# Kernel optimization log

Hardware: AMD Instinct MI355X
Metric: run time of the kernel (lower is better)

The kernel has to match this reference:

```python
import jax, jax.numpy as jnp
import numpy as np
from jax import lax

B, C, T, H, HEAD, NC = 256, 64, 2048, 64, 32, 8

def setup_inputs() -> dict:
    key = jax.random.key(0)
    ks = jax.random.split(key, 20)
    s = 0.08
    d = {}
    d["x"] = jax.random.normal(ks[0], (B, C, T), jnp.float32)
    # GRU layer 0: input C -> hidden H (gates order r,z,n as in PyTorch)
    d["w_ih0"] = jax.random.normal(ks[1], (3 * H, C), jnp.float32) * s
    d["w_hh0"] = jax.random.normal(ks[2], (3 * H, H), jnp.float32) * s
    d["b_ih0"] = jax.random.normal(ks[3], (3 * H,), jnp.float32) * s
    d["b_hh0"] = jax.random.normal(ks[4], (3 * H,), jnp.float32) * s
    # GRU layer 1: H -> H
    d["w_ih1"] = jax.random.normal(ks[5], (3 * H, H), jnp.float32) * s
    d["w_hh1"] = jax.random.normal(ks[6], (3 * H, H), jnp.float32) * s
    d["b_ih1"] = jax.random.normal(ks[7], (3 * H,), jnp.float32) * s
    d["b_hh1"] = jax.random.normal(ks[8], (3 * H,), jnp.float32) * s
    # additive attention: Linear(H,H) -> tanh -> Linear(H,1)
    d["attn_w1"] = jax.random.normal(ks[9], (H, H), jnp.float32) * s
    d["attn_b1"] = jax.random.normal(ks[10], (H,), jnp.float32) * s
    d["attn_w2"] = jax.random.normal(ks[11], (1, H), jnp.float32) * s
    d["attn_b2"] = jax.random.normal(ks[12], (1,), jnp.float32) * s
    # head: LayerNorm(H) -> Linear(H,32) -> GELU -> Linear(32,NC)
    d["ln_g"] = jnp.ones((H,), jnp.float32)
    d["ln_b"] = jnp.zeros((H,), jnp.float32)
    d["head_w1"] = jax.random.normal(ks[13], (HEAD, H), jnp.float32) * s
    d["head_b1"] = jax.random.normal(ks[14], (HEAD,), jnp.float32) * s
    d["head_w2"] = jax.random.normal(ks[15], (NC, HEAD), jnp.float32) * s
    d["head_b2"] = jax.random.normal(ks[16], (NC,), jnp.float32) * s
    return d


def _gru_layer(x, w_ih, w_hh, b_ih, b_hh):
    # x: (B, T, F) -> (B, T, H). PyTorch GRU cell math, gate order r,z,n.
    bsz = x.shape[0]
    hid = w_hh.shape[1]
    # precompute input contributions for all timesteps in one big GEMM
    xg = jnp.einsum('btf,gf->btg', x, w_ih) + b_ih  # (B, T, 3H)
    xg = jnp.swapaxes(xg, 0, 1)  # (T, B, 3H)

    def step(h, xg_t):
        hg = h @ w_hh.T + b_hh  # (B, 3H)
        xr, xz, xn = jnp.split(xg_t, 3, axis=-1)
        hr, hz, hn = jnp.split(hg, 3, axis=-1)
        r = jax.nn.sigmoid(xr + hr)
        z = jax.nn.sigmoid(xz + hz)
        n = jnp.tanh(xn + r * hn)
        h_new = (1.0 - z) * n + z * h
        return h_new, h_new

    h0 = jnp.zeros((bsz, hid), x.dtype)
    _, hs = lax.scan(step, h0, xg)  # hs: (T, B, H)
    return jnp.swapaxes(hs, 0, 1)


def _forward(x, w_ih0, w_hh0, b_ih0, b_hh0, w_ih1, w_hh1, b_ih1, b_hh1,
             attn_w1, attn_b1, attn_w2, attn_b2, ln_g, ln_b,
             head_w1, head_b1, head_w2, head_b2):
    xt = jnp.swapaxes(x, 1, 2)  # (B, T, C)
    h = _gru_layer(xt, w_ih0, w_hh0, b_ih0, b_hh0)
    h = _gru_layer(h, w_ih1, w_hh1, b_ih1, b_hh1)  # (B, T, H)
    # additive attention pooling
    a = jnp.tanh(jnp.einsum('bth,oh->bto', h, attn_w1) + attn_b1)
    w = jnp.einsum('bth,oh->bto', a, attn_w2)[..., 0] + attn_b2[0]  # (B, T)
    w = jax.nn.softmax(w, axis=-1)
    pooled = jnp.einsum('bth,bt->bh', h, w)  # (B, H)
    # LayerNorm (eps=1e-5 as in torch)
    mu = jnp.mean(pooled, axis=-1, keepdims=True)
    var = jnp.mean(jnp.square(pooled - mu), axis=-1, keepdims=True)
    y = (pooled - mu) * lax.rsqrt(var + 1e-5) * ln_g + ln_b
    y = jax.nn.gelu(y @ head_w1.T + head_b1, approximate=False)
    return y @ head_w2.T + head_b2  # (B, NC)


def reference(x, w_ih0, w_hh0, b_ih0, b_hh0, w_ih1, w_hh1, b_ih1, b_hh1,
              attn_w1, attn_b1, attn_w2, attn_b2, ln_g, ln_b,
              head_w1, head_b1, head_w2, head_b2):
    return _forward(x, w_ih0, w_hh0, b_ih0, b_hh0, w_ih1, w_hh1, b_ih1, b_hh1,
                    attn_w1, attn_b1, attn_w2, attn_b2, ln_g, ln_b,
                    head_w1, head_b1, head_w2, head_b2)
```

## Files before the change

### kernel.cpp

```cpp
#include <hip/hip_runtime.h>
#include <math.h>

#define TS 2048

typedef float f32x2 __attribute__((ext_vector_type(2)));
typedef _Float16 f16;
typedef _Float16 f16x2 __attribute__((ext_vector_type(2)));
typedef _Float16 f16x8 __attribute__((ext_vector_type(8)));

#define XG0_B  5120
#define XG1_B  8192
#define H0H_B  11264
#define H1H_B  12288
#define H1F_B  12800
#define SCRO_B 13824
#define LDSF   13920

#define BAR() do { asm volatile("s_waitcnt lgkmcnt(0)" ::: "memory"); __builtin_amdgcn_s_barrier(); } while(0)
#define FEN() asm volatile("s_waitcnt lgkmcnt(0)" ::: "memory")

union H8 { f16x8 v8; f16x2 v2[4]; };

__device__ __forceinline__ float sigmoidf_(float v){ return __builtin_amdgcn_rcpf(1.0f+__expf(-v)); }
__device__ __forceinline__ float tanhf_(float v){
  v = fminf(15.0f, fmaxf(-15.0f, v));
  const float e = __expf(2.0f*v);
  return (e-1.0f)*__builtin_amdgcn_rcpf(e+1.0f);
}
__device__ __forceinline__ float qadd1(float v){
  return v + __int_as_float(__builtin_amdgcn_update_dpp(0, __float_as_int(v), 0xB1, 0xF, 0xF, true));
}
__device__ __forceinline__ float wsum64(float v){
  v += __int_as_float(__builtin_amdgcn_update_dpp(0, __float_as_int(v), 0x111, 0xF, 0xF, true));
  v += __int_as_float(__builtin_amdgcn_update_dpp(0, __float_as_int(v), 0x112, 0xF, 0xF, true));
  v += __int_as_float(__builtin_amdgcn_update_dpp(0, __float_as_int(v), 0x114, 0xF, 0xF, true));
  v += __int_as_float(__builtin_amdgcn_update_dpp(0, __float_as_int(v), 0x118, 0xF, 0xF, true));
  v += __int_as_float(__builtin_amdgcn_update_dpp(0, __float_as_int(v), 0x142, 0xA, 0xF, true));
  v += __int_as_float(__builtin_amdgcn_update_dpp(0, __float_as_int(v), 0x143, 0xC, 0xF, true));
  return __int_as_float(__builtin_amdgcn_readlane(__float_as_int(v), 63));
}
__device__ __forceinline__ float fdot2_(f16x2 a, f16x2 b, float c){
  return __builtin_amdgcn_fdot2(a, b, c, false);
}
__device__ __forceinline__ void dot6(const f16* vec, const f16x2* Wp,
                                     float& a00, float& a01, float& a02,
                                     float& a10, float& a11, float& a12){
  H8 u[4];
  u[0].v8 = *(const f16x8*)(vec);
  u[1].v8 = *(const f16x8*)(vec+8);
  u[2].v8 = *(const f16x8*)(vec+16);
  u[3].v8 = *(const f16x8*)(vec+24);
  #pragma unroll
  for (int m=0;m<16;m++){
    const f16x2 hm = u[m>>2].v2[m&3];
    a00 = fdot2_(Wp[m],    hm, a00);
    a01 = fdot2_(Wp[16+m], hm, a01);
    a02 = fdot2_(Wp[32+m], hm, a02);
    a10 = fdot2_(Wp[48+m], hm, a10);
    a11 = fdot2_(Wp[64+m], hm, a11);
    a12 = fdot2_(Wp[80+m], hm, a12);
  }
}

__global__ __launch_bounds__(448, 1)
void gru_attn_fused(const float* __restrict__ x,
                    const float* __restrict__ w_ih0, const float* __restrict__ w_hh0,
                    const float* __restrict__ b_ih0, const float* __restrict__ b_hh0,
                    const float* __restrict__ w_ih1, const float* __restrict__ w_hh1,
                    const float* __restrict__ b_ih1, const float* __restrict__ b_hh1,
                    const float* __restrict__ attn_w1, const float* __restrict__ attn_b1,
                    const float* __restrict__ attn_w2, const float* __restrict__ attn_b2,
                    const float* __restrict__ ln_g, const float* __restrict__ ln_b,
                    const float* __restrict__ head_w1, const float* __restrict__ head_b1,
                    const float* __restrict__ head_w2, const float* __restrict__ head_b2,
                    float* __restrict__ out)
{
  __shared__ float lds[LDSF];
  f16*   ldsx = (f16*)lds;
  float* xg0  = lds + XG0_B;
  float* xg1  = lds + XG1_B;
  f16*   h0h  = (f16*)(lds + H0H_B);
  f16*   h1h  = (f16*)(lds + H1H_B);
  float* h1f  = lds + H1F_B;

  const int tid  = threadIdx.x;
  const int wid  = tid >> 6;
  const int lane = tid & 63;
  const int b    = blockIdx.x;
  const float* xb = x + (size_t)b * 64 * TS;

  const int i2     = lane >> 1;
  const int p      = lane & 1;
  const int ownrow = i2 + 32*p;
  const int hoff   = p << 5;

  f16x2 W[96];
  float4 SP[16];
  float bA=0.f,bB=0.f,bC=0.f,w2o=0.f,b2v=0.f;

  if (wid < 4) {
    const float* wsrc = (wid==0)? w_hh0 : (wid==1)? w_hh1 : (wid==2)? w_ih1 : w_ih0;
    for (int r2=0;r2<2;r2++)
      for (int g=0;g<3;g++)
        for (int m=0;m<16;m++){
          const f32x2 v = *(const f32x2*)(wsrc + (size_t)(g*64 + i2 + 32*r2)*64 + hoff + 2*m);
          W[(r2*3+g)*16+m] = (f16x2){(f16)v.x,(f16)v.y};
        }
    for (int q2=0;q2<96;q2++) asm volatile("" : "+v"(W[q2]));
    const float* bsrc = (wid==0)? b_hh0 : (wid==1)? b_hh1 : (wid==2)? b_ih1 : b_ih0;
    bA = bsrc[ownrow]; bB = bsrc[64+ownrow]; bC = bsrc[128+ownrow];
  } else if (wid == 6) {
    for (int r2=0;r2<2;r2++)
      for (int m=0;m<16;m++){
        const f32x2 v = *(const f32x2*)(attn_w1 + (size_t)(i2+32*r2)*64 + hoff + 2*m);
        W[r2*16+m] = (f16x2){(f16)v.x,(f16)v.y};
      }
    for (int q2=0;q2<32;q2++) asm volatile("" : "+v"(W[q2]));
    bA = attn_b1[ownrow]; w2o = attn_w2[ownrow]; b2v = attn_b2[0];
  }

  for (int idx = tid; idx < 1024; idx += 448) ((uint32_t*)h0h)[idx] = 0u;
  for (int idx = tid; idx < 512;  idx += 448) ((uint32_t*)h1h)[idx] = 0u;
  if (wid == 4) {
    const float* src = xb + (size_t)lane*TS;
    #pragma unroll
    for (int kq=0;kq<16;kq++) SP[kq] = *(const float4*)(src + 4*kq);
    #pragma unroll
    for (int kq=0;kq<16;kq++){
      ldsx[(4*kq+0)*80 + lane] = (f16)SP[kq].x;
      ldsx[(4*kq+1)*80 + lane] = (f16)SP[kq].y;
      ldsx[(4*kq+2)*80 + lane] = (f16)SP[kq].z;
      ldsx[(4*kq+3)*80 + lane] = (f16)SP[kq].w;
    }
  }
  __syncthreads();

  if (wid <= 1) __builtin_amdgcn_s_setprio(1);

  float hreg = 0.f;
  float am = -1e30f, aZ = 0.f, aP = 0.f;

  #pragma unroll 1
  for (int k = -1; k <= 258; ++k) {
    if (wid <= 1) {
      const int blk = k - (wid << 1);
      if (0 <= blk && blk < 256) {
        f16*   hring = wid ? h1h : h0h;
        float* xgc   = wid ? xg1 : xg0;
        const int emask = wid ? 1023 : 2047;
        const int t0 = blk << 3;
        float xgr = xgc[(t0&15)*192 + ownrow];
        float xgz = xgc[(t0&15)*192 + 64 + ownrow];
        float xgn = xgc[(t0&15)*192 + 128 + ownrow];
        #pragma unroll
        for (int j=0;j<8;j++){
          const int t = t0 + j;
          FEN();
          const f16* hv = hring + (((t-1)<<6) & emask) + hoff;
          float a00=0,a01=0,a02=0,a10=0,a11=0,a12=0;
          dot6(hv, W, a00,a01,a02,a10,a11,a12);
          a00=qadd1(a00); a01=qadd1(a01); a02=qadd1(a02);
          a10=qadd1(a10); a11=qadd1(a11); a12=qadd1(a12);
          const float hr = p ? a10 : a00;
          const float hz = p ? a11 : a01;
          const float hn = p ? a12 : a02;
          const float r = sigmoidf_(xgr + hr + bA);
          const float z = sigmoidf_(xgz + hz + bB);
          const float n = tanhf_(xgn + r*(hn + bC));
          hreg = n + z*(hreg - n);
          hring[((t<<6) & emask) + ownrow] = (f16)hreg;
          if (wid) h1f[((t&15)<<6) + ownrow] = hreg;
          if (j < 7) {
            const int xi = ((t+1)&15)*192;
            xgr = xgc[xi + ownrow];
            xgz = xgc[xi + 64 + ownrow];
            xgn = xgc[xi + 128 + ownrow];
          }
        }
      }
    } else if (wid <= 3) {
      const int blk = (wid==2) ? k-1 : k+1;
      if (0 <= blk && blk < 256) {
        float* xgw = (wid==2) ? xg1 : xg0;
        #pragma unroll
        for (int j=0;j<8;j++){
          const int t = (blk<<3) + j;
          const f16* vec;
          if (wid==2) vec = h0h + (((t-1)<<6) & 2047) + hoff;
          else        vec = ldsx + ((t>>6)&1)*5120 + (t&63)*80 + hoff;
          float a00=0,a01=0,a02=0,a10=0,a11=0,a12=0;
          dot6(vec, W, a00,a01,a02,a10,a11,a12);
          a00=qadd1(a00); a01=qadd1(a01); a02=qadd1(a02);
          a10=qadd1(a10); a11=qadd1(a11); a12=qadd1(a12);
          const int xi = (t & 15) * 192;
          xgw[xi + ownrow]       = (p ? a10 : a00) + bA;
          xgw[xi + 64 + ownrow]  = (p ? a11 : a01) + bB;
          xgw[xi + 128 + ownrow] = (p ? a12 : a02) + bC;
        }
      }
    } else if (wid == 4) {
      const int kk = k + 1, tile = kk >> 3, ph = kk & 7;
      if (ph == 1 && tile < 31) {
        const float* src = xb + (size_t)lane*TS + (tile+1)*64;
        #pragma unroll
        for (int kq=0;kq<16;kq++) SP[kq] = *(const float4*)(src + 4*kq);
      } else if (ph == 5 && tile < 31) {
        f16* dsth = ldsx + ((tile+1)&1)*5120;
        #pragma unroll
        for (int kq=0;kq<16;kq++){
          dsth[(4*kq+0)*80 + lane] = (f16)SP[kq].x;
          dsth[(4*kq+1)*80 + lane] = (f16)SP[kq].y;
          dsth[(4*kq+2)*80 + lane] = (f16)SP[kq].z;
          dsth[(4*kq+3)*80 + lane] = (f16)SP[kq].w;
        }
      }
    } else if (wid == 6) {
      const int blk = k - 3;
      if (0 <= blk && blk < 256) {
        #pragma unroll
        for (int j=0;j<8;j++){
          const int t = (blk<<3) + j;
          const f16* hv = h1h + ((t&15)<<6) + hoff;
          H8 u[4];
          u[0].v8 = *(const f16x8*)(hv);
          u[1].v8 = *(const f16x8*)(hv+8);
          u[2].v8 = *(const f16x8*)(hv+16);
          u[3].v8 = *(const f16x8*)(hv+24);
          float a0=0.f, a1=0.f;
          #pragma unroll
          for (int m=0;m<16;m++){
            const f16x2 hm = u[m>>2].v2[m&3];
            a0 = fdot2_(W[m],    hm, a0);
            a1 = fdot2_(W[16+m], hm, a1);
          }
          a0 = qadd1(a0); a1 = qadd1(a1);
          const float a  = tanhf_((p ? a1 : a0) + bA);
          const float s  = wsum64(w2o * a) + b2v;
          const float hc = h1f[((t&15)<<6) + lane];
          const float mn = fmaxf(am, s);
          const float sc = __expf(am - mn);
          const float pp = __expf(s - mn);
          aZ = aZ*sc + pp;
          aP = aP*sc + pp*hc;
          am = mn;
        }
      }
    }
    BAR();
  }

  if (wid == 6) {
    const float pooled = aP / aZ;
    float mu = pooled;
    #pragma unroll
    for (int m=1;m<64;m<<=1) mu += __shfl_xor(mu, m, 64);
    mu *= (1.0f/64.0f);
    const float d = pooled - mu;
    float var = d*d;
    #pragma unroll
    for (int m=1;m<64;m<<=1) var += __shfl_xor(var, m, 64);
    var *= (1.0f/64.0f);
    const float y = d * rsqrtf(var + 1e-5f) * ln_g[lane] + ln_b[lane];
    lds[SCRO_B + lane] = y;
  }
  __syncthreads();
  if (tid < 32) {
    const float* hw = head_w1 + tid*64;
    float acc = head_b1[tid];
    #pragma unroll
    for (int kq=0;kq<16;kq++){
      const float4 w4 = ((const float4*)hw)[kq];
      acc += w4.x*lds[SCRO_B+4*kq+0] + w4.y*lds[SCRO_B+4*kq+1]
           + w4.z*lds[SCRO_B+4*kq+2] + w4.w*lds[SCRO_B+4*kq+3];
    }
    const float u = 0.5f*acc*(1.0f + erff(acc*0.70710678118654752f));
    lds[SCRO_B + 64 + tid] = u;
  }
  __syncthreads();
  if (tid < 8) {
    const float* hw = head_w2 + tid*32;
    float acc = head_b2[tid];
    #pragma unroll
    for (int kq=0;kq<8;kq++){
      const float4 w4 = ((const float4*)hw)[kq];
      acc += w4.x*lds[SCRO_B+64+4*kq+0] + w4.y*lds[SCRO_B+64+4*kq+1]
           + w4.z*lds[SCRO_B+64+4*kq+2] + w4.w*lds[SCRO_B+64+4*kq+3];
    }
    out[b*8 + tid] = acc;
  }
}

extern "C" void kernel_launch(void* const* d_in, const int* in_sizes, int n_in,
                              void* d_out, int out_size, void* d_ws, size_t ws_size,
                              hipStream_t stream) {
  (void)in_sizes; (void)n_in; (void)d_ws; (void)ws_size; (void)out_size;
  const float* x       = (const float*)d_in[0];
  const float* w_ih0   = (const float*)d_in[1];
  const float* w_hh0   = (const float*)d_in[2];
  const float* b_ih0   = (const float*)d_in[3];
  const float* b_hh0   = (const float*)d_in[4];
  const float* w_ih1   = (const float*)d_in[5];
  const float* w_hh1   = (const float*)d_in[6];
  const float* b_ih1   = (const float*)d_in[7];
  const float* b_hh1   = (const float*)d_in[8];
  const float* attn_w1 = (const float*)d_in[9];
  const float* attn_b1 = (const float*)d_in[10];
  const float* attn_w2 = (const float*)d_in[11];
  const float* attn_b2 = (const float*)d_in[12];
  const float* ln_g    = (const float*)d_in[13];
  const float* ln_b    = (const float*)d_in[14];
  const float* head_w1 = (const float*)d_in[15];
  const float* head_b1 = (const float*)d_in[16];
  const float* head_w2 = (const float*)d_in[17];
  const float* head_b2 = (const float*)d_in[18];
  hipLaunchKernelGGL(gru_attn_fused, dim3(256), dim3(448), 0, stream,
                     x, w_ih0, w_hh0, b_ih0, b_hh0, w_ih1, w_hh1, b_ih1, b_hh1,
                     attn_w1, attn_b1, attn_w2, attn_b2, ln_g, ln_b,
                     head_w1, head_b1, head_w2, head_b2, (float*)d_out);
}
```

Before: 793.9 us.

## Pack two batch elements per block with twelve waves sharing the CU

Result: slower. 1.354 ms (+70.5%).

```diff
diff --git a/kernel.cpp b/kernel.cpp
--- a/kernel.cpp
+++ b/kernel.cpp
@@ -2,6 +2,7 @@
 #include <math.h>
 
 #define TS 2048
+#define PB 13920
 
 typedef float f32x2 __attribute__((ext_vector_type(2)));
 typedef _Float16 f16;
@@ -14,7 +15,6 @@
 #define H1H_B  12288
 #define H1F_B  12800
 #define SCRO_B 13824
-#define LDSF   13920
 
 #define BAR() do { asm volatile("s_waitcnt lgkmcnt(0)" ::: "memory"); __builtin_amdgcn_s_barrier(); } while(0)
 #define FEN() asm volatile("s_waitcnt lgkmcnt(0)" ::: "memory")
@@ -62,7 +62,7 @@
   }
 }
 
-__global__ __launch_bounds__(448, 1)
+__global__ __launch_bounds__(768, 1)
 void gru_attn_fused(const float* __restrict__ x,
                     const float* __restrict__ w_ih0, const float* __restrict__ w_hh0,
                     const float* __restrict__ b_ih0, const float* __restrict__ b_hh0,
@@ -75,31 +75,34 @@
                     const float* __restrict__ head_w2, const float* __restrict__ head_b2,
                     float* __restrict__ out)
 {
-  __shared__ float lds[LDSF];
-  f16*   ldsx = (f16*)lds;
-  float* xg0  = lds + XG0_B;
-  float* xg1  = lds + XG1_B;
-  f16*   h0h  = (f16*)(lds + H0H_B);
-  f16*   h1h  = (f16*)(lds + H1H_B);
-  float* h1f  = lds + H1F_B;
-
+  __shared__ float lds[2*PB];
   const int tid  = threadIdx.x;
   const int wid  = tid >> 6;
   const int lane = tid & 63;
-  const int b    = blockIdx.x;
-  const float* xb = x + (size_t)b * 64 * TS;
+  const int blkx = blockIdx.x;
+  const int be   = (wid >= 6);
+  const int rl   = be ? wid-6 : wid;
+
+  float* ldsb = lds + be*PB;
+  f16*   ldsx = (f16*)ldsb;
+  float* xg0  = ldsb + XG0_B;
+  float* xg1  = ldsb + XG1_B;
+  f16*   h0h  = (f16*)(ldsb + H0H_B);
+  f16*   h1h  = (f16*)(ldsb + H1H_B);
+  float* h1f  = ldsb + H1F_B;
 
   const int i2     = lane >> 1;
   const int p      = lane & 1;
   const int ownrow = i2 + 32*p;
   const int hoff   = p << 5;
+  const float* xb  = x + (size_t)(2*blkx + be) * 64 * TS;
 
   f16x2 W[96];
   float4 SP[16];
   float bA=0.f,bB=0.f,bC=0.f,w2o=0.f,b2v=0.f;
 
-  if (wid < 4) {
-    const float* wsrc = (wid==0)? w_hh0 : (wid==1)? w_hh1 : (wid==2)? w_ih1 : w_ih0;
+  if (rl < 4) {
+    const float* wsrc = (rl==0)? w_hh0 : (rl==1)? w_hh1 : (rl==2)? w_ih1 : w_ih0;
     for (int r2=0;r2<2;r2++)
       for (int g=0;g<3;g++)
         for (int m=0;m<16;m++){
@@ -107,9 +110,9 @@
           W[(r2*3+g)*16+m] = (f16x2){(f16)v.x,(f16)v.y};
         }
     for (int q2=0;q2<96;q2++) asm volatile("" : "+v"(W[q2]));
-    const float* bsrc = (wid==0)? b_hh0 : (wid==1)? b_hh1 : (wid==2)? b_ih1 : b_ih0;
+    const float* bsrc = (rl==0)? b_hh0 : (rl==1)? b_hh1 : (rl==2)? b_ih1 : b_ih0;
     bA = bsrc[ownrow]; bB = bsrc[64+ownrow]; bC = bsrc[128+ownrow];
-  } else if (wid == 6) {
+  } else if (rl == 5) {
     for (int r2=0;r2<2;r2++)
       for (int m=0;m<16;m++){
         const f32x2 v = *(const f32x2*)(attn_w1 + (size_t)(i2+32*r2)*64 + hoff + 2*m);
@@ -119,9 +122,9 @@
     bA = attn_b1[ownrow]; w2o = attn_w2[ownrow]; b2v = attn_b2[0];
   }
 
-  for (int idx = tid; idx < 1024; idx += 448) ((uint32_t*)h0h)[idx] = 0u;
-  for (int idx = tid; idx < 512;  idx += 448) ((uint32_t*)h1h)[idx] = 0u;
-  if (wid == 4) {
+  for (int idx = tid; idx < 1536; idx += 768) ((uint32_t*)(lds + H0H_B))[idx] = 0u;
+  for (int idx = tid; idx < 1536; idx += 768) ((uint32_t*)(lds + PB + H0H_B))[idx] = 0u;
+  if (rl == 4) {
     const float* src = xb + (size_t)lane*TS;
     #pragma unroll
     for (int kq=0;kq<16;kq++) SP[kq] = *(const float4*)(src + 4*kq);
@@ -135,19 +138,19 @@
   }
   __syncthreads();
 
-  if (wid <= 1) __builtin_amdgcn_s_setprio(1);
+  if (rl <= 1) __builtin_amdgcn_s_setprio(1);
 
   float hreg = 0.f;
   float am = -1e30f, aZ = 0.f, aP = 0.f;
 
   #pragma unroll 1
   for (int k = -1; k <= 258; ++k) {
-    if (wid <= 1) {
-      const int blk = k - (wid << 1);
+    if (rl <= 1) {
+      const int blk = k - (rl << 1);
       if (0 <= blk && blk < 256) {
-        f16*   hring = wid ? h1h : h0h;
-        float* xgc   = wid ? xg1 : xg0;
-        const int emask = wid ? 1023 : 2047;
+        f16*   hring = rl ? h1h : h0h;
+        float* xgc   = rl ? xg1 : xg0;
+        const int emask = rl ? 1023 : 2047;
         const int t0 = blk << 3;
         float xgr = xgc[(t0&15)*192 + ownrow];
         float xgz = xgc[(t0&15)*192 + 64 + ownrow];
@@ -169,7 +172,7 @@
           const float n = tanhf_(xgn + r*(hn + bC));
           hreg = n + z*(hreg - n);
           hring[((t<<6) & emask) + ownrow] = (f16)hreg;
-          if (wid) h1f[((t&15)<<6) + ownrow] = hreg;
+          if (rl) h1f[((t&15)<<6) + ownrow] = hreg;
           if (j < 7) {
             const int xi = ((t+1)&15)*192;
             xgr = xgc[xi + ownrow];
@@ -178,16 +181,16 @@
           }
         }
       }
-    } else if (wid <= 3) {
-      const int blk = (wid==2) ? k-1 : k+1;
+    } else if (rl <= 3) {
+      const int blk = (rl==2) ? k-1 : k+1;
       if (0 <= blk && blk < 256) {
-        float* xgw = (wid==2) ? xg1 : xg0;
+        float* xgw = (rl==2) ? xg1 : xg0;
         #pragma unroll
         for (int j=0;j<8;j++){
           const int t = (blk<<3) + j;
           const f16* vec;
-          if (wid==2) vec = h0h + (((t-1)<<6) & 2047) + hoff;
-          else        vec = ldsx + ((t>>6)&1)*5120 + (t&63)*80 + hoff;
+          if (rl==2) vec = h0h + (((t-1)<<6) & 2047) + hoff;
+          else       vec = ldsx + ((t>>6)&1)*5120 + (t&63)*80 + hoff;
           float a00=0,a01=0,a02=0,a10=0,a11=0,a12=0;
           dot6(vec, W, a00,a01,a02,a10,a11,a12);
           a00=qadd1(a00); a01=qadd1(a01); a02=qadd1(a02);
@@ -198,7 +201,7 @@
           xgw[xi + 128 + ownrow] = (p ? a12 : a02) + bC;
         }
       }
-    } else if (wid == 4) {
+    } else if (rl == 4) {
       const int kk = k + 1, tile = kk >> 3, ph = kk & 7;
       if (ph == 1 && tile < 31) {
         const float* src = xb + (size_t)lane*TS + (tile+1)*64;
@@ -214,7 +217,7 @@
           dsth[(4*kq+3)*80 + lane] = (f16)SP[kq].w;
         }
       }
-    } else if (wid == 6) {
+    } else {
       const int blk = k - 3;
       if (0 <= blk && blk < 256) {
         #pragma unroll
@@ -249,7 +252,7 @@
     BAR();
   }
 
-  if (wid == 6) {
+  if (rl == 5) {
     const float pooled = aP / aZ;
     float mu = pooled;
     #pragma unroll
@@ -261,32 +264,32 @@
     for (int m=1;m<64;m<<=1) var += __shfl_xor(var, m, 64);
     var *= (1.0f/64.0f);
     const float y = d * rsqrtf(var + 1e-5f) * ln_g[lane] + ln_b[lane];
-    lds[SCRO_B + lane] = y;
+    ldsb[SCRO_B + lane] = y;
   }
   __syncthreads();
-  if (tid < 32) {
-    const float* hw = head_w1 + tid*64;
-    float acc = head_b1[tid];
+  if (rl == 0 && lane < 32) {
+    const float* hw = head_w1 + lane*64;
+    float acc = head_b1[lane];
     #pragma unroll
     for (int kq=0;kq<16;kq++){
       const float4 w4 = ((const float4*)hw)[kq];
-      acc += w4.x*lds[SCRO_B+4*kq+0] + w4.y*lds[SCRO_B+4*kq+1]
-           + w4.z*lds[SCRO_B+4*kq+2] + w4.w*lds[SCRO_B+4*kq+3];
+      acc += w4.x*ldsb[SCRO_B+4*kq+0] + w4.y*ldsb[SCRO_B+4*kq+1]
+           + w4.z*ldsb[SCRO_B+4*kq+2] + w4.w*ldsb[SCRO_B+4*kq+3];
     }
     const float u = 0.5f*acc*(1.0f + erff(acc*0.70710678118654752f));
-    lds[SCRO_B + 64 + tid] = u;
+    ldsb[SCRO_B + 64 + lane] = u;
   }
   __syncthreads();
-  if (tid < 8) {
-    const float* hw = head_w2 + tid*32;
-    float acc = head_b2[tid];
+  if (rl == 0 && lane < 8) {
+    const float* hw = head_w2 + lane*32;
+    float acc = head_b2[lane];
     #pragma unroll
     for (int kq=0;kq<8;kq++){
       const float4 w4 = ((const float4*)hw)[kq];
-      acc += w4.x*lds[SCRO_B+64+4*kq+0] + w4.y*lds[SCRO_B+64+4*kq+1]
-           + w4.z*lds[SCRO_B+64+4*kq+2] + w4.w*lds[SCRO_B+64+4*kq+3];
+      acc += w4.x*ldsb[SCRO_B+64+4*kq+0] + w4.y*ldsb[SCRO_B+64+4*kq+1]
+           + w4.z*ldsb[SCRO_B+64+4*kq+2] + w4.w*ldsb[SCRO_B+64+4*kq+3];
     }
-    out[b*8 + tid] = acc;
+    out[(size_t)(2*blkx + be)*8 + lane] = acc;
   }
 }
 
@@ -313,7 +316,7 @@
   const float* head_b1 = (const float*)d_in[16];
   const float* head_w2 = (const float*)d_in[17];
   const float* head_b2 = (const float*)d_in[18];
-  hipLaunchKernelGGL(gru_attn_fused, dim3(256), dim3(448), 0, stream,
+  hipLaunchKernelGGL(gru_attn_fused, dim3(128), dim3(768), 0, stream,
                      x, w_ih0, w_hh0, b_ih0, b_hh0, w_ih1, w_hh1, b_ih1, b_hh1,
                      attn_w1, attn_b1, attn_w2, attn_b2, ln_g, ln_b,
                      head_w1, head_b1, head_w2, head_b2, (float*)d_out);
```
